# Kernel optimization log

Hardware: AMD Instinct MI355X
Metric: run time of the kernel (lower is better)

Reference implementation:

```python
import jax, jax.numpy as jnp
import numpy as np

N, D, H, O = 200000, 256, 256, 128


def _linear_params(key, fan_in, fan_out):
    # matches torch.nn.Linear default init: U(-1/sqrt(fan_in), 1/sqrt(fan_in))
    lim = 1.0 / np.sqrt(fan_in)
    kw, kb = jax.random.split(key)
    W = jax.random.uniform(kw, (fan_in, fan_out), minval=-lim, maxval=lim, dtype=jnp.float32)
    b = jax.random.uniform(kb, (fan_out,), minval=-lim, maxval=lim, dtype=jnp.float32)
    return W, b


def setup_inputs() -> dict:
    key = jax.random.key(0)
    ks = jax.random.split(key, 6)
    node_embeddings = jax.random.normal(ks[0], (N, D), dtype=jnp.float32)
    # adjacency_list keys: all < N so every key is 'valid'
    adj_keys = jax.random.randint(ks[1], (N,), 0, N, dtype=jnp.int64) if jax.config.jax_enable_x64 else jax.random.randint(ks[1], (N,), 0, N, dtype=jnp.int32)
    W1, b1 = _linear_params(ks[2], D, H)
    W2, b2 = _linear_params(ks[3], H, H)
    W3, b3 = _linear_params(ks[4], H, H)
    Wo, bo = _linear_params(ks[5], H, O)
    return {
        "node_embeddings": node_embeddings,
        "adj_keys": adj_keys,
        "W1": W1, "b1": b1,
        "W2": W2, "b2": b2,
        "W3": W3, "b3": b3,
        "Wo": Wo, "bo": bo,
    }


def reference(node_embeddings, adj_keys, W1, b1, W2, b2, W3, b3, Wo, bo):
    # --- aggregation path (faithful to the torch code's actual math) ---
    # All adj_keys are < N, so valid_indices == keys and the re-enumeration
    # `mapping` makes `indices` exactly arange(num_keys).
    indices = jnp.arange(adj_keys.shape[0])
    neighbors = node_embeddings[indices]              # [N, D] row gather
    # torch.mean(row, dim=0) on a 1-D row == scalar mean over features
    aggregated_embeddings = jnp.mean(neighbors, axis=1)  # [N]

    # --- dense 3-layer SAGE MLP + output projection ---
    x = jax.nn.relu(node_embeddings @ W1 + b1)        # [N, H]
    x = jax.nn.relu(x @ W2 + b2)                      # [N, H]
    x = jax.nn.relu(x @ W3 + b3)                      # [N, H]
    x = x @ Wo + bo                                   # [N, O]
    return (x, aggregated_embeddings)
```

## Files before the change

kernel.cpp:

```cpp
#include <hip/hip_runtime.h>
#include <hip/hip_bf16.h>
#include <cstdint>


#define N_ROWS 200000
#define O_DIM  128
#define ROWS   64
#define PITCH  264

typedef short bf16x8 __attribute__((ext_vector_type(8)));
typedef float f32x4  __attribute__((ext_vector_type(4)));

__device__ __forceinline__ unsigned short rne_bf16(float f) {
  unsigned int u = __float_as_uint(f);
  u += 0x7FFFu + ((u >> 16) & 1u);
  return (unsigned short)(u >> 16);
}

__global__ __launch_bounds__(256) void prep_kernel(
    const float* __restrict__ W1, const float* __restrict__ W2,
    const float* __restrict__ W3, const float* __restrict__ Wo,
    unsigned short* __restrict__ wt) {
  const int b = blockIdx.x;
  const int t = threadIdx.x;
  if (b < 256) {
    wt[b * 256 + t] = rne_bf16(W1[t * 256 + b]);
  } else if (b < 512) {
    const int o = b - 256;
    wt[65536 + o * 256 + t] = rne_bf16(W2[t * 256 + o]);
  } else if (b < 768) {
    const int o = b - 512;
    wt[131072 + o * 256 + t] = rne_bf16(W3[t * 256 + o]);
  } else {
    const int o = b - 768;
    wt[196608 + o * 256 + t] = rne_bf16(Wo[t * 128 + o]);
  }
}

template <int MB, bool RELU, bool LAST>
__device__ __forceinline__ void do_layer(
    const unsigned short* __restrict__ wt, const float* __restrict__ bias,
    float* __restrict__ out_x, long row0, unsigned short* act,
    int wave, int lane) {
  const int lc   = lane & 15;
  const int quad = lane >> 4;
  const int m_base = wave * (MB * 16);

  f32x4 acc[MB][4];
#pragma unroll
  for (int mb = 0; mb < MB; ++mb)
#pragma unroll
    for (int nb = 0; nb < 4; ++nb)
      acc[mb][nb] = (f32x4){0.f, 0.f, 0.f, 0.f};

#pragma unroll
  for (int k0 = 0; k0 < 256; k0 += 32) {
    bf16x8 bfr[4];
#pragma unroll
    for (int nb = 0; nb < 4; ++nb)
      bfr[nb] = *(const bf16x8*)&act[(nb * 16 + lc) * PITCH + k0 + 8 * quad];
#pragma unroll
    for (int mb = 0; mb < MB; ++mb) {
      bf16x8 afr = *(const bf16x8*)&wt[(m_base + mb * 16 + lc) * 256 + k0 + 8 * quad];
#pragma unroll
      for (int nb = 0; nb < 4; ++nb)
        acc[mb][nb] = __builtin_amdgcn_mfma_f32_16x16x32_bf16(afr, bfr[nb],
                                                              acc[mb][nb], 0, 0, 0);
    }
  }
  __syncthreads();

#pragma unroll
  for (int mb = 0; mb < MB; ++mb) {
    const int ch = m_base + mb * 16 + 4 * quad;
    f32x4 bb = *(const f32x4*)(bias + ch);
#pragma unroll
    for (int nb = 0; nb < 4; ++nb) {
      f32x4 v = acc[mb][nb] + bb;
      if (RELU) {
#pragma unroll
        for (int j = 0; j < 4; ++j) v[j] = fmaxf(v[j], 0.f);
      }
      const int r = nb * 16 + lc;
      if (!LAST) {
        ushort4 h;
        h.x = rne_bf16(v[0]); h.y = rne_bf16(v[1]);
        h.z = rne_bf16(v[2]); h.w = rne_bf16(v[3]);
        *(ushort4*)&act[r * PITCH + ch] = h;
      } else {
        const long gr = row0 + r;
        *(f32x4*)&out_x[gr * O_DIM + ch] = v;
      }
    }
  }
  __syncthreads();
}

__global__ __launch_bounds__(256, 4) void sage_kernel(
    const float* __restrict__ E,
    const float* __restrict__ b1, const float* __restrict__ b2,
    const float* __restrict__ b3, const float* __restrict__ bo,
    const unsigned short* __restrict__ wts,
    float* __restrict__ out_x, float* __restrict__ out_agg) {
  __shared__ __align__(16) unsigned short act[ROWS * PITCH];

  const int t    = threadIdx.x;
  const int wave = t >> 6;
  const int lane = t & 63;
  const long row0 = (long)blockIdx.x * ROWS;

  f32x4 v[16];
#pragma unroll
  for (int i = 0; i < 16; ++i) {
    const int r = 4 * i + wave;
    v[i] = *(const f32x4*)(E + (row0 + r) * 256 + lane * 4);
  }

#pragma unroll
  for (int i = 0; i < 16; ++i) {
    const int r = 4 * i + wave;
    const long gr = row0 + r;
    ushort4 h;
    h.x = rne_bf16(v[i][0]); h.y = rne_bf16(v[i][1]);
    h.z = rne_bf16(v[i][2]); h.w = rne_bf16(v[i][3]);
    *(ushort4*)&act[r * PITCH + lane * 4] = h;
    float s = v[i][0] + v[i][1] + v[i][2] + v[i][3];
    s += __shfl_down(s, 32);
    s += __shfl_down(s, 16);
    s += __shfl_down(s, 8);
    s += __shfl_down(s, 4);
    s += __shfl_down(s, 2);
    s += __shfl_down(s, 1);
    if (lane == 0) out_agg[gr] = s * (1.0f / 256.0f);
  }
  __syncthreads();

  do_layer<4, true,  false>(wts,          b1, nullptr, row0, act, wave, lane);
  do_layer<4, true,  false>(wts + 65536,  b2, nullptr, row0, act, wave, lane);
  do_layer<4, true,  false>(wts + 131072, b3, nullptr, row0, act, wave, lane);
  do_layer<2, false, true >(wts + 196608, bo, out_x,   row0, act, wave, lane);
}

extern "C" void kernel_launch(void* const* d_in, const int* in_sizes, int n_in,
                              void* d_out, int out_size, void* d_ws, size_t ws_size,
                              hipStream_t stream) {
  const float* E  = (const float*)d_in[0];
  const float* W1 = (const float*)d_in[2];
  const float* b1 = (const float*)d_in[3];
  const float* W2 = (const float*)d_in[4];
  const float* b2 = (const float*)d_in[5];
  const float* W3 = (const float*)d_in[6];
  const float* b3 = (const float*)d_in[7];
  const float* Wo = (const float*)d_in[8];
  const float* bo = (const float*)d_in[9];

  float* out_x   = (float*)d_out;
  float* out_agg = out_x + (size_t)N_ROWS * O_DIM;
  unsigned short* wts = (unsigned short*)d_ws;

  prep_kernel<<<896, 256, 0, stream>>>(W1, W2, W3, Wo, wts);

  const int grid = N_ROWS / ROWS;
  sage_kernel<<<grid, 256, 0, stream>>>(E, b1, b2, b3, bo, wts, out_x, out_agg);
}
```

Before: 513.4 us.

## Make sage kernel persistent with next-tile prefetch and double-buffered fragments

```diff
diff --git a/kernel.cpp b/kernel.cpp
--- a/kernel.cpp
+++ b/kernel.cpp
@@ -7,6 +7,8 @@
 #define O_DIM  128
 #define ROWS   64
 #define PITCH  264
+#define NTILES 3125
+#define GRID   512
 
 typedef short bf16x8 __attribute__((ext_vector_type(8)));
 typedef float f32x4  __attribute__((ext_vector_type(4)));
@@ -37,11 +39,11 @@
   }
 }
 
-template <int MB, bool RELU, bool LAST>
+template <int MB, bool RELU, bool LAST, bool PF>
 __device__ __forceinline__ void do_layer(
     const unsigned short* __restrict__ wt, const float* __restrict__ bias,
     float* __restrict__ out_x, long row0, unsigned short* act,
-    int wave, int lane) {
+    int wave, int lane, const float* __restrict__ Enext, f32x4* stage) {
   const int lc   = lane & 15;
   const int quad = lane >> 4;
   const int m_base = wave * (MB * 16);
@@ -53,20 +55,37 @@
     for (int nb = 0; nb < 4; ++nb)
       acc[mb][nb] = (f32x4){0.f, 0.f, 0.f, 0.f};
 
-#pragma unroll
-  for (int k0 = 0; k0 < 256; k0 += 32) {
-    bf16x8 bfr[4];
-#pragma unroll
-    for (int nb = 0; nb < 4; ++nb)
-      bfr[nb] = *(const bf16x8*)&act[(nb * 16 + lc) * PITCH + k0 + 8 * quad];
-#pragma unroll
-    for (int mb = 0; mb < MB; ++mb) {
-      bf16x8 afr = *(const bf16x8*)&wt[(m_base + mb * 16 + lc) * 256 + k0 + 8 * quad];
+  bf16x8 a[2][MB], b[2][4];
+#pragma unroll
+  for (int nb = 0; nb < 4; ++nb)
+    b[0][nb] = *(const bf16x8*)&act[(nb * 16 + lc) * PITCH + 8 * quad];
+#pragma unroll
+  for (int mb = 0; mb < MB; ++mb)
+    a[0][mb] = *(const bf16x8*)&wt[(m_base + mb * 16 + lc) * 256 + 8 * quad];
+
+#pragma unroll
+  for (int ks = 0; ks < 8; ++ks) {
+    const int cur = ks & 1, nxt = cur ^ 1;
+    if (PF) {
+      const int i0 = 2 * ks;
+      stage[i0]     = *(const f32x4*)(Enext + (i0 * 4 + wave) * 256 + lane * 4);
+      stage[i0 + 1] = *(const f32x4*)(Enext + ((i0 + 1) * 4 + wave) * 256 + lane * 4);
+    }
+    if (ks < 7) {
+      const int k0 = (ks + 1) * 32;
 #pragma unroll
       for (int nb = 0; nb < 4; ++nb)
-        acc[mb][nb] = __builtin_amdgcn_mfma_f32_16x16x32_bf16(afr, bfr[nb],
+        b[nxt][nb] = *(const bf16x8*)&act[(nb * 16 + lc) * PITCH + k0 + 8 * quad];
+#pragma unroll
+      for (int mb = 0; mb < MB; ++mb)
+        a[nxt][mb] = *(const bf16x8*)&wt[(m_base + mb * 16 + lc) * 256 + k0 + 8 * quad];
+    }
+#pragma unroll
+    for (int mb = 0; mb < MB; ++mb)
+#pragma unroll
+      for (int nb = 0; nb < 4; ++nb)
+        acc[mb][nb] = __builtin_amdgcn_mfma_f32_16x16x32_bf16(a[cur][mb], b[cur][nb],
                                                               acc[mb][nb], 0, 0, 0);
-    }
   }
   __syncthreads();
 
@@ -89,14 +108,14 @@
         *(ushort4*)&act[r * PITCH + ch] = h;
       } else {
         const long gr = row0 + r;
-        *(f32x4*)&out_x[gr * O_DIM + ch] = v;
+        __builtin_nontemporal_store(v, (f32x4*)&out_x[gr * O_DIM + ch]);
       }
     }
   }
   __syncthreads();
 }
 
-__global__ __launch_bounds__(256, 4) void sage_kernel(
+__global__ __launch_bounds__(256, 2) void sage_kernel(
     const float* __restrict__ E,
     const float* __restrict__ b1, const float* __restrict__ b2,
     const float* __restrict__ b3, const float* __restrict__ bo,
@@ -107,38 +126,59 @@
   const int t    = threadIdx.x;
   const int wave = t >> 6;
   const int lane = t & 63;
-  const long row0 = (long)blockIdx.x * ROWS;
-
-  f32x4 v[16];
-#pragma unroll
-  for (int i = 0; i < 16; ++i) {
-    const int r = 4 * i + wave;
-    v[i] = *(const f32x4*)(E + (row0 + r) * 256 + lane * 4);
-  }
-
-#pragma unroll
-  for (int i = 0; i < 16; ++i) {
-    const int r = 4 * i + wave;
-    const long gr = row0 + r;
-    ushort4 h;
-    h.x = rne_bf16(v[i][0]); h.y = rne_bf16(v[i][1]);
-    h.z = rne_bf16(v[i][2]); h.w = rne_bf16(v[i][3]);
-    *(ushort4*)&act[r * PITCH + lane * 4] = h;
-    float s = v[i][0] + v[i][1] + v[i][2] + v[i][3];
-    s += __shfl_down(s, 32);
-    s += __shfl_down(s, 16);
-    s += __shfl_down(s, 8);
-    s += __shfl_down(s, 4);
-    s += __shfl_down(s, 2);
-    s += __shfl_down(s, 1);
-    if (lane == 0) out_agg[gr] = s * (1.0f / 256.0f);
-  }
-  __syncthreads();
-
-  do_layer<4, true,  false>(wts,          b1, nullptr, row0, act, wave, lane);
-  do_layer<4, true,  false>(wts + 65536,  b2, nullptr, row0, act, wave, lane);
-  do_layer<4, true,  false>(wts + 131072, b3, nullptr, row0, act, wave, lane);
-  do_layer<2, false, true >(wts + 196608, bo, out_x,   row0, act, wave, lane);
+
+  f32x4 stage[16];
+
+  int tile = blockIdx.x;
+  {
+    const float* Ep = E + (long)tile * ROWS * 256;
+#pragma unroll
+    for (int i = 0; i < 16; ++i)
+      stage[i] = *(const f32x4*)(Ep + (i * 4 + wave) * 256 + lane * 4);
+  }
+
+  while (true) {
+    const long row0 = (long)tile * ROWS;
+
+#pragma unroll
+    for (int i = 0; i < 16; ++i) {
+      const int r = i * 4 + wave;
+      ushort4 h;
+      h.x = rne_bf16(stage[i][0]); h.y = rne_bf16(stage[i][1]);
+      h.z = rne_bf16(stage[i][2]); h.w = rne_bf16(stage[i][3]);
+      *(ushort4*)&act[r * PITCH + lane * 4] = h;
+      float s = stage[i][0] + stage[i][1] + stage[i][2] + stage[i][3];
+      s += __shfl_down(s, 32);
+      s += __shfl_down(s, 16);
+      s += __shfl_down(s, 8);
+      s += __shfl_down(s, 4);
+      s += __shfl_down(s, 2);
+      s += __shfl_down(s, 1);
+      if (lane == 0)
+        __builtin_nontemporal_store(s * (1.0f / 256.0f), &out_agg[row0 + r]);
+    }
+    __syncthreads();
+
+    const int next = tile + GRID;
+    const bool has_next = next < NTILES;
+    const float* Enext = E + (long)next * ROWS * 256;
+
+    if (has_next)
+      do_layer<4, true, false, true >(wts, b1, nullptr, row0, act, wave, lane,
+                                      Enext, stage);
+    else
+      do_layer<4, true, false, false>(wts, b1, nullptr, row0, act, wave, lane,
+                                      nullptr, stage);
+    do_layer<4, true,  false, false>(wts + 65536,  b2, nullptr, row0, act, wave,
+                                     lane, nullptr, stage);
+    do_layer<4, true,  false, false>(wts + 131072, b3, nullptr, row0, act, wave,
+                                     lane, nullptr, stage);
+    do_layer<2, false, true,  false>(wts + 196608, bo, out_x,   row0, act, wave,
+                                     lane, nullptr, stage);
+
+    if (!has_next) break;
+    tile = next;
+  }
 }
 
 extern "C" void kernel_launch(void* const* d_in, const int* in_sizes, int n_in,
@@ -160,6 +200,5 @@
 
   prep_kernel<<<896, 256, 0, stream>>>(W1, W2, W3, Wo, wts);
 
-  const int grid = N_ROWS / ROWS;
-  sage_kernel<<<grid, 256, 0, stream>>>(E, b1, b2, b3, bo, wts, out_x, out_agg);
-}
+  sage_kernel<<<GRID, 256, 0, stream>>>(E, b1, b2, b3, bo, wts, out_x, out_agg);
+}
```

After: 626.0 us. +21.9%, slower.

## Persistent kernel with double-buffered LDS weight staging and swizzled layout

Applied to the files above, without the earlier changes.

```diff
diff --git a/kernel.cpp b/kernel.cpp
--- a/kernel.cpp
+++ b/kernel.cpp
@@ -6,7 +6,8 @@
 #define N_ROWS 200000
 #define O_DIM  128
 #define ROWS   64
-#define PITCH  264
+#define NTILES 3125
+#define GRIDP  256
 
 typedef short bf16x8 __attribute__((ext_vector_type(8)));
 typedef float f32x4  __attribute__((ext_vector_type(4)));
@@ -16,6 +17,8 @@
   u += 0x7FFFu + ((u >> 16) & 1u);
   return (unsigned short)(u >> 16);
 }
+
+__device__ __forceinline__ int swz(int b) { return b ^ (((b >> 9) & 7) << 4); }
 
 __global__ __launch_bounds__(256) void prep_kernel(
     const float* __restrict__ W1, const float* __restrict__ W2,
@@ -37,108 +40,156 @@
   }
 }
 
-template <int MB, bool RELU, bool LAST>
-__device__ __forceinline__ void do_layer(
-    const unsigned short* __restrict__ wt, const float* __restrict__ bias,
-    float* __restrict__ out_x, long row0, unsigned short* act,
-    int wave, int lane) {
-  const int lc   = lane & 15;
-  const int quad = lane >> 4;
-  const int m_base = wave * (MB * 16);
-
-  f32x4 acc[MB][4];
-#pragma unroll
-  for (int mb = 0; mb < MB; ++mb)
+template <bool FILL>
+__device__ __forceinline__ void half_mm(
+    const unsigned short* __restrict__ wslot, const char* __restrict__ actb,
+    bf16x8 bc[8][4], f32x4 acc[4], int wave, int lc, int quad) {
+  const char* wb = (const char*)wslot;
+#pragma unroll
+  for (int ks = 0; ks < 8; ++ks) {
+    const int k0 = ks * 32;
+    const bf16x8 afr =
+        *(const bf16x8*)(wb + swz((wave * 16 + lc) * 512 + k0 * 2 + 16 * quad));
+    if (FILL) {
+#pragma unroll
+      for (int nb = 0; nb < 4; ++nb)
+        bc[ks][nb] = *(const bf16x8*)(actb +
+                       swz((nb * 16 + lc) * 512 + k0 * 2 + 16 * quad));
+    }
 #pragma unroll
     for (int nb = 0; nb < 4; ++nb)
-      acc[mb][nb] = (f32x4){0.f, 0.f, 0.f, 0.f};
-
-#pragma unroll
-  for (int k0 = 0; k0 < 256; k0 += 32) {
-    bf16x8 bfr[4];
-#pragma unroll
-    for (int nb = 0; nb < 4; ++nb)
-      bfr[nb] = *(const bf16x8*)&act[(nb * 16 + lc) * PITCH + k0 + 8 * quad];
-#pragma unroll
-    for (int mb = 0; mb < MB; ++mb) {
-      bf16x8 afr = *(const bf16x8*)&wt[(m_base + mb * 16 + lc) * 256 + k0 + 8 * quad];
-#pragma unroll
-      for (int nb = 0; nb < 4; ++nb)
-        acc[mb][nb] = __builtin_amdgcn_mfma_f32_16x16x32_bf16(afr, bfr[nb],
-                                                              acc[mb][nb], 0, 0, 0);
-    }
-  }
-  __syncthreads();
-
-#pragma unroll
-  for (int mb = 0; mb < MB; ++mb) {
-    const int ch = m_base + mb * 16 + 4 * quad;
-    f32x4 bb = *(const f32x4*)(bias + ch);
+      acc[nb] = __builtin_amdgcn_mfma_f32_16x16x32_bf16(afr, bc[ks][nb],
+                                                        acc[nb], 0, 0, 0);
+  }
+}
+
+__device__ __forceinline__ void layer_store_act(
+    char* __restrict__ actb, const float* __restrict__ bias,
+    f32x4 acc0[4], f32x4 acc1[4], int wave, int lc, int quad) {
+#pragma unroll
+  for (int h = 0; h < 2; ++h) {
+    f32x4* acc = h ? acc1 : acc0;
+    const int ch = h * 128 + wave * 16 + 4 * quad;
+    const f32x4 bb = *(const f32x4*)(bias + ch);
 #pragma unroll
     for (int nb = 0; nb < 4; ++nb) {
-      f32x4 v = acc[mb][nb] + bb;
-      if (RELU) {
-#pragma unroll
-        for (int j = 0; j < 4; ++j) v[j] = fmaxf(v[j], 0.f);
-      }
+      f32x4 v = acc[nb] + bb;
+#pragma unroll
+      for (int j = 0; j < 4; ++j) v[j] = fmaxf(v[j], 0.f);
       const int r = nb * 16 + lc;
-      if (!LAST) {
-        ushort4 h;
-        h.x = rne_bf16(v[0]); h.y = rne_bf16(v[1]);
-        h.z = rne_bf16(v[2]); h.w = rne_bf16(v[3]);
-        *(ushort4*)&act[r * PITCH + ch] = h;
-      } else {
-        const long gr = row0 + r;
-        *(f32x4*)&out_x[gr * O_DIM + ch] = v;
-      }
-    }
-  }
-  __syncthreads();
-}
-
-__global__ __launch_bounds__(256, 4) void sage_kernel(
+      ushort4 hq;
+      hq.x = rne_bf16(v[0]); hq.y = rne_bf16(v[1]);
+      hq.z = rne_bf16(v[2]); hq.w = rne_bf16(v[3]);
+      *(ushort4*)(actb + swz(r * 512 + ch * 2)) = hq;
+    }
+  }
+}
+
+__global__ __launch_bounds__(512, 2) void sage_kernel(
     const float* __restrict__ E,
     const float* __restrict__ b1, const float* __restrict__ b2,
     const float* __restrict__ b3, const float* __restrict__ bo,
     const unsigned short* __restrict__ wts,
     float* __restrict__ out_x, float* __restrict__ out_agg) {
-  __shared__ __align__(16) unsigned short act[ROWS * PITCH];
+  __shared__ __align__(16) unsigned short act[16384];
+  __shared__ __align__(16) unsigned short wbuf[2][32768];
+  char* actb = (char*)act;
 
   const int t    = threadIdx.x;
   const int wave = t >> 6;
   const int lane = t & 63;
-  const long row0 = (long)blockIdx.x * ROWS;
-
-  f32x4 v[16];
-#pragma unroll
-  for (int i = 0; i < 16; ++i) {
-    const int r = 4 * i + wave;
-    v[i] = *(const f32x4*)(E + (row0 + r) * 256 + lane * 4);
-  }
-
-#pragma unroll
-  for (int i = 0; i < 16; ++i) {
-    const int r = 4 * i + wave;
-    const long gr = row0 + r;
-    ushort4 h;
-    h.x = rne_bf16(v[i][0]); h.y = rne_bf16(v[i][1]);
-    h.z = rne_bf16(v[i][2]); h.w = rne_bf16(v[i][3]);
-    *(ushort4*)&act[r * PITCH + lane * 4] = h;
-    float s = v[i][0] + v[i][1] + v[i][2] + v[i][3];
-    s += __shfl_down(s, 32);
-    s += __shfl_down(s, 16);
-    s += __shfl_down(s, 8);
-    s += __shfl_down(s, 4);
-    s += __shfl_down(s, 2);
-    s += __shfl_down(s, 1);
-    if (lane == 0) out_agg[gr] = s * (1.0f / 256.0f);
-  }
-  __syncthreads();
-
-  do_layer<4, true,  false>(wts,          b1, nullptr, row0, act, wave, lane);
-  do_layer<4, true,  false>(wts + 65536,  b2, nullptr, row0, act, wave, lane);
-  do_layer<4, true,  false>(wts + 131072, b3, nullptr, row0, act, wave, lane);
-  do_layer<2, false, true >(wts + 196608, bo, out_x,   row0, act, wave, lane);
+  const int lc   = lane & 15;
+  const int quad = lane >> 4;
+
+  auto stage_issue = [&](const unsigned short* wsrc, unsigned short* slot) {
+#pragma unroll
+    for (int rnd = 0; rnd < 8; ++rnd) {
+      const int lds_rel = rnd * 8192 + wave * 1024 + lane * 16;
+      __builtin_amdgcn_global_load_lds(
+          (const unsigned int*)((const char*)wsrc + swz(lds_rel)),
+          (unsigned int*)((char*)slot + rnd * 8192 + wave * 1024),
+          16, 0, 0);
+    }
+  };
+
+  bf16x8 bc[8][4];
+  f32x4 acc0[4], acc1[4];
+
+  int tile = blockIdx.x;
+  stage_issue(wts, wbuf[0]);
+  int sel = 1;
+
+  for (;;) {
+    const long row0 = (long)tile * ROWS;
+
+    __syncthreads();
+
+    {
+      f32x4 st[8];
+#pragma unroll
+      for (int i = 0; i < 8; ++i)
+        st[i] = *(const f32x4*)(E + (row0 + i * 8 + wave) * 256 + lane * 4);
+#pragma unroll
+      for (int i = 0; i < 8; ++i) {
+        const int r = i * 8 + wave;
+        ushort4 h;
+        h.x = rne_bf16(st[i][0]); h.y = rne_bf16(st[i][1]);
+        h.z = rne_bf16(st[i][2]); h.w = rne_bf16(st[i][3]);
+        *(ushort4*)(actb + swz(r * 512 + lane * 8)) = h;
+        float s = st[i][0] + st[i][1] + st[i][2] + st[i][3];
+        s += __shfl_down(s, 32);
+        s += __shfl_down(s, 16);
+        s += __shfl_down(s, 8);
+        s += __shfl_down(s, 4);
+        s += __shfl_down(s, 2);
+        s += __shfl_down(s, 1);
+        if (lane == 0) out_agg[row0 + r] = s * (1.0f / 256.0f);
+      }
+    }
+    __syncthreads();
+
+    const unsigned short* wl = wts;
+    const float* bias[3] = {b1, b2, b3};
+#pragma unroll 1
+    for (int L = 0; L < 3; ++L) {
+      stage_issue(wl + 32768, wbuf[sel]);
+#pragma unroll
+      for (int nb = 0; nb < 4; ++nb) acc0[nb] = (f32x4){0.f, 0.f, 0.f, 0.f};
+      half_mm<true>(wbuf[sel ^ 1], actb, bc, acc0, wave, lc, quad);
+      __syncthreads();
+      sel ^= 1;
+
+      stage_issue(L < 2 ? wl + 65536 : wts + 196608, wbuf[sel]);
+#pragma unroll
+      for (int nb = 0; nb < 4; ++nb) acc1[nb] = (f32x4){0.f, 0.f, 0.f, 0.f};
+      half_mm<false>(wbuf[sel ^ 1], actb, bc, acc1, wave, lc, quad);
+      layer_store_act(actb, bias[L], acc0, acc1, wave, lc, quad);
+      __syncthreads();
+      sel ^= 1;
+      wl += 65536;
+    }
+
+    const int nxt = tile + GRIDP;
+    const bool has_next = nxt < NTILES;
+    if (has_next) stage_issue(wts, wbuf[sel]);
+#pragma unroll
+    for (int nb = 0; nb < 4; ++nb) acc0[nb] = (f32x4){0.f, 0.f, 0.f, 0.f};
+    half_mm<true>(wbuf[sel ^ 1], actb, bc, acc0, wave, lc, quad);
+    sel ^= 1;
+    {
+      const int ch = wave * 16 + 4 * quad;
+      const f32x4 bb = *(const f32x4*)(bo + ch);
+#pragma unroll
+      for (int nb = 0; nb < 4; ++nb) {
+        f32x4 v = acc0[nb] + bb;
+        const long gr = row0 + nb * 16 + lc;
+        *(f32x4*)&out_x[gr * O_DIM + ch] = v;
+      }
+    }
+
+    if (!has_next) break;
+    tile = nxt;
+  }
 }
 
 extern "C" void kernel_launch(void* const* d_in, const int* in_sizes, int n_in,
@@ -160,6 +211,5 @@
 
   prep_kernel<<<896, 256, 0, stream>>>(W1, W2, W3, Wo, wts);
 
-  const int grid = N_ROWS / ROWS;
-  sage_kernel<<<grid, 256, 0, stream>>>(E, b1, b2, b3, bo, wts, out_x, out_agg);
-}
+  sage_kernel<<<GRIDP, 512, 0, stream>>>(E, b1, b2, b3, bo, wts, out_x, out_agg);
+}
```

Result: slower. 523.8 us (+2.0%).
